# Performance work log

Hardware: AMD Instinct MI355X
Metric: run time of the kernel (lower is better)

The kernel has to match this reference:

```python
import jax, jax.numpy as jnp
import numpy as np

D_MODEL = 1024
NHEAD = 16
HEAD_DIM = D_MODEL // NHEAD
SCALE = 1.0 / float(np.sqrt(HEAD_DIM))


def setup_inputs() -> dict:
    key = jax.random.key(0)
    ks = jax.random.split(key, 9)
    B, S = 1, 4096
    s = 1.0 / float(np.sqrt(D_MODEL))
    inp = {
        "x": jax.random.normal(ks[0], (B, S, D_MODEL), dtype=jnp.float32),
        "Wq": jax.random.uniform(ks[1], (D_MODEL, D_MODEL), jnp.float32, -s, s),
        "bq": jax.random.uniform(ks[2], (D_MODEL,), jnp.float32, -s, s),
        "Wk": jax.random.uniform(ks[3], (D_MODEL, D_MODEL), jnp.float32, -s, s),
        "bk": jax.random.uniform(ks[4], (D_MODEL,), jnp.float32, -s, s),
        "Wv": jax.random.uniform(ks[5], (D_MODEL, D_MODEL), jnp.float32, -s, s),
        "bv": jax.random.uniform(ks[6], (D_MODEL,), jnp.float32, -s, s),
        "Wo": jax.random.uniform(ks[7], (D_MODEL, D_MODEL), jnp.float32, -s, s),
        "bo": jax.random.uniform(ks[8], (D_MODEL,), jnp.float32, -s, s),
    }
    return inp


def reference(x, Wq, bq, Wk, bk, Wv, bv, Wo, bo):
    B, S, _ = x.shape
    # projections (torch Linear: y = x @ W.T + b)
    q = x @ Wq.T + bq
    k = x @ Wk.T + bk
    v = x @ Wv.T + bv
    # [B, H, S, Dh]
    q = q.reshape(B, S, NHEAD, HEAD_DIM).transpose(0, 2, 1, 3)
    k = k.reshape(B, S, NHEAD, HEAD_DIM).transpose(0, 2, 1, 3)
    v = v.reshape(B, S, NHEAD, HEAD_DIM).transpose(0, 2, 1, 3)
    # [B, H, S, S] scores with causal mask
    scores = jnp.einsum("bhsd,bhtd->bhst", q, k) * SCALE
    causal = jnp.triu(jnp.ones((S, S), dtype=bool), k=1)
    scores = jnp.where(causal, -jnp.inf, scores)
    attn = jax.nn.softmax(scores, axis=-1)
    out = jnp.einsum("bhst,bhtd->bhsd", attn, v)
    out = out.transpose(0, 2, 1, 3).reshape(B, S, D_MODEL)
    return out @ Wo.T + bo
```

## Files before the change

kernel.cpp:

```cpp
#include <hip/hip_runtime.h>

typedef unsigned short u16;
typedef unsigned int u32;
typedef short bf16x8 __attribute__((ext_vector_type(8)));
typedef float f32x4 __attribute__((ext_vector_type(4)));
typedef float f32x16 __attribute__((ext_vector_type(16)));
typedef u32 u32x4 __attribute__((ext_vector_type(4)));

#define S_LEN 4096
#define DM 1024
#define NH 16
#define DH 64
#define CE 0.18033688f
#define THR 8.0f

typedef const __attribute__((address_space(1))) u32 gu32;
typedef __attribute__((address_space(3))) u32 lu32;

#define EXP2(x) __builtin_amdgcn_exp2f(x)

__device__ __forceinline__ u16 f2bf(float f) {
  u32 u = __builtin_bit_cast(u32, f);
  u += 0x7fff + ((u >> 16) & 1);
  return (u16)(u >> 16);
}

__device__ __forceinline__ f32x16 zero16() {
  f32x16 z;
#pragma unroll
  for (int i = 0; i < 16; ++i) z[i] = 0.f;
  return z;
}

__device__ __forceinline__ u32 cvt_pk_bf16(float lo, float hi) {
  u32 r;
  asm("v_cvt_pk_bf16_f32 %0, %1, %2" : "=v"(r) : "v"(lo), "v"(hi));
  return r;
}

__device__ __forceinline__ void pl_swap(u32& a, u32& b) {
  asm("v_permlane32_swap_b32 %0, %1" : "+v"(a), "+v"(b));
}

__global__ void cvt_bf16(const float* __restrict__ in, u16* __restrict__ out, int n4) {
  int i = blockIdx.x * blockDim.x + threadIdx.x;
  if (i < n4) {
    float4 v = ((const float4*)in)[i];
    ushort4 o;
    o.x = f2bf(v.x); o.y = f2bf(v.y); o.z = f2bf(v.z); o.w = f2bf(v.w);
    ((ushort4*)out)[i] = o;
  }
}

__global__ void cvt_bf16_w4(const float* __restrict__ a, const float* __restrict__ b,
                            const float* __restrict__ c, const float* __restrict__ d,
                            u16* __restrict__ oa, u16* __restrict__ ob2,
                            u16* __restrict__ oc, u16* __restrict__ od, int n4) {
  const int w = blockIdx.y;
  const float* src = (w == 0) ? a : (w == 1) ? b : (w == 2) ? c : d;
  u16* dst = (w == 0) ? oa : (w == 1) ? ob2 : (w == 2) ? oc : od;
  int i = blockIdx.x * blockDim.x + threadIdx.x;
  if (i < n4) {
    float4 v = ((const float4*)src)[i];
    ushort4 o;
    o.x = f2bf(v.x); o.y = f2bf(v.y); o.z = f2bf(v.z); o.w = f2bf(v.w);
    ((ushort4*)dst)[i] = o;
  }
}

__global__ __launch_bounds__(256) void gemm_qkv(const u16* __restrict__ A,
                                                const u16* __restrict__ Wq_, const u16* __restrict__ Wk_, const u16* __restrict__ Wv_,
                                                const float* __restrict__ bq_, const float* __restrict__ bk_, const float* __restrict__ bv_,
                                                u16* __restrict__ Qo, u16* __restrict__ Ko, u16* __restrict__ Vo) {
  __shared__ __align__(16) u16 As[128 * 32];
  __shared__ __align__(16) u16 Bs[128 * 32];
  const int z = blockIdx.z;
  const u16* Bt = (z == 0) ? Wq_ : (z == 1) ? Wk_ : Wv_;
  const float* bias = (z == 0) ? bq_ : (z == 1) ? bk_ : bv_;

  const int tid = threadIdx.x;
  const int lane = tid & 63;
  const int wid = tid >> 6;
  const int wm = wid >> 1, wn = wid & 1;
  const int bm = blockIdx.x * 128, bn = blockIdx.y * 128;
  const int lr = lane & 15, lg = lane >> 4;

  f32x4 acc[4][4];
#pragma unroll
  for (int i = 0; i < 4; ++i)
#pragma unroll
    for (int j = 0; j < 4; ++j) acc[i][j] = f32x4{0.f, 0.f, 0.f, 0.f};

  const int r0 = tid >> 2;
  const int c0 = (tid & 3) * 8;
  const u16* ga0 = A + (size_t)(bm + r0) * DM + c0;
  const u16* gb0 = Bt + (size_t)(bn + r0) * DM + c0;

  for (int kt = 0; kt < DM; kt += 32) {
    __builtin_amdgcn_global_load_lds((gu32*)(ga0 + kt),            (lu32*)(As + tid * 8),        16, 0, 0);
    __builtin_amdgcn_global_load_lds((gu32*)(ga0 + 64 * DM + kt),  (lu32*)(As + 2048 + tid * 8), 16, 0, 0);
    __builtin_amdgcn_global_load_lds((gu32*)(gb0 + kt),            (lu32*)(Bs + tid * 8),        16, 0, 0);
    __builtin_amdgcn_global_load_lds((gu32*)(gb0 + 64 * DM + kt),  (lu32*)(Bs + 2048 + tid * 8), 16, 0, 0);
    __syncthreads();
    bf16x8 af[4], bfr[4];
#pragma unroll
    for (int i = 0; i < 4; ++i) af[i] = *(const bf16x8*)&As[(wm * 64 + i * 16 + lr) * 32 + lg * 8];
#pragma unroll
    for (int j = 0; j < 4; ++j) bfr[j] = *(const bf16x8*)&Bs[(wn * 64 + j * 16 + lr) * 32 + lg * 8];
#pragma unroll
    for (int i = 0; i < 4; ++i)
#pragma unroll
      for (int j = 0; j < 4; ++j)
        acc[i][j] = __builtin_amdgcn_mfma_f32_16x16x32_bf16(af[i], bfr[j], acc[i][j], 0, 0, 0);
    __syncthreads();
  }

#pragma unroll
  for (int i = 0; i < 4; ++i) {
    const int row = bm + wm * 64 + i * 16 + lg * 4;
#pragma unroll
    for (int j = 0; j < 4; ++j) {
      const int col = bn + wn * 64 + j * 16 + lr;
      const float b = bias[col];
#pragma unroll
      for (int r = 0; r < 4; ++r) {
        const float v = acc[i][j][r] + b;
        const int s = row + r;
        if (z == 0) {
          Qo[(size_t)s * DM + col] = f2bf(v * CE);
        } else if (z == 1) {
          const int hh = col >> 6, c = col & 63;
          Ko[(size_t)hh * (S_LEN * 64) + (size_t)(s >> 5) * 2048 +
             (c >> 4) * 512 + ((c >> 3) & 1) * 256 + (s & 31) * 8 + (c & 7)] = f2bf(v);
        } else {
          const int hh = col >> 6, dl = col & 63;
          const int kl = s & 31;
          Vo[(size_t)hh * (S_LEN * 64) + (size_t)(s >> 5) * 2048 +
             ((dl >> 5) * 2 + (kl >> 4)) * 512 +
             ((((kl >> 3) & 1) * 32 + (dl & 31)) * 8) + (kl & 7)] = f2bf(v);
        }
      }
    }
  }
}

__global__ __launch_bounds__(256) void gemm_out(const u16* __restrict__ A,
                                                const u16* __restrict__ Bt,
                                                const float* __restrict__ bias,
                                                float* __restrict__ Cp) {
  __shared__ __align__(16) u16 As[128 * 32];
  __shared__ __align__(16) u16 Bs[128 * 32];
  const int tid = threadIdx.x;
  const int lane = tid & 63;
  const int wid = tid >> 6;
  const int wm = wid >> 1, wn = wid & 1;
  const int bm = blockIdx.x * 128, bn = blockIdx.y * 128;
  const int lr = lane & 15, lg = lane >> 4;

  f32x4 acc[4][4];
#pragma unroll
  for (int i = 0; i < 4; ++i)
#pragma unroll
    for (int j = 0; j < 4; ++j) acc[i][j] = f32x4{0.f, 0.f, 0.f, 0.f};

  const int r0 = tid >> 2;
  const int c0 = (tid & 3) * 8;
  const u16* ga0 = A + (size_t)(bm + r0) * DM + c0;
  const u16* gb0 = Bt + (size_t)(bn + r0) * DM + c0;

  for (int kt = 0; kt < DM; kt += 32) {
    __builtin_amdgcn_global_load_lds((gu32*)(ga0 + kt),            (lu32*)(As + tid * 8),        16, 0, 0);
    __builtin_amdgcn_global_load_lds((gu32*)(ga0 + 64 * DM + kt),  (lu32*)(As + 2048 + tid * 8), 16, 0, 0);
    __builtin_amdgcn_global_load_lds((gu32*)(gb0 + kt),            (lu32*)(Bs + tid * 8),        16, 0, 0);
    __builtin_amdgcn_global_load_lds((gu32*)(gb0 + 64 * DM + kt),  (lu32*)(Bs + 2048 + tid * 8), 16, 0, 0);
    __syncthreads();
    bf16x8 af[4], bfr[4];
#pragma unroll
    for (int i = 0; i < 4; ++i) af[i] = *(const bf16x8*)&As[(wm * 64 + i * 16 + lr) * 32 + lg * 8];
#pragma unroll
    for (int j = 0; j < 4; ++j) bfr[j] = *(const bf16x8*)&Bs[(wn * 64 + j * 16 + lr) * 32 + lg * 8];
#pragma unroll
    for (int i = 0; i < 4; ++i)
#pragma unroll
      for (int j = 0; j < 4; ++j)
        acc[i][j] = __builtin_amdgcn_mfma_f32_16x16x32_bf16(af[i], bfr[j], acc[i][j], 0, 0, 0);
    __syncthreads();
  }

#pragma unroll
  for (int i = 0; i < 4; ++i) {
    const int row = bm + wm * 64 + i * 16 + lg * 4;
#pragma unroll
    for (int j = 0; j < 4; ++j) {
      const int col = bn + wn * 64 + j * 16 + lr;
      const float b = bias[col];
#pragma unroll
      for (int r = 0; r < 4; ++r)
        Cp[(size_t)(row + r) * DM + col] = acc[i][j][r] + b;
    }
  }
}


__device__ __forceinline__ void ld_kt(const u16* __restrict__ tb, bf16x8* kf) {
  kf[0] = *(const bf16x8*)&tb[0];
  kf[1] = *(const bf16x8*)&tb[512];
  kf[2] = *(const bf16x8*)&tb[1024];
  kf[3] = *(const bf16x8*)&tb[1536];
}

template<bool DIAG>
__device__ __forceinline__ void attn_tile32(const bf16x8* kf, const bf16x8* vf,
                                            const bf16x8* qf, int lld,
                                            f32x16& o0, f32x16& o1,
                                            float& m, float& lsum) {
  f32x16 s = zero16();
  __builtin_amdgcn_s_setprio(1);
  s = __builtin_amdgcn_mfma_f32_32x32x16_bf16(kf[0], qf[0], s, 0, 0, 0);
  s = __builtin_amdgcn_mfma_f32_32x32x16_bf16(kf[1], qf[1], s, 0, 0, 0);
  s = __builtin_amdgcn_mfma_f32_32x32x16_bf16(kf[2], qf[2], s, 0, 0, 0);
  s = __builtin_amdgcn_mfma_f32_32x32x16_bf16(kf[3], qf[3], s, 0, 0, 0);
  __builtin_amdgcn_s_setprio(0);

  float p[16];
#pragma unroll
  for (int r = 0; r < 16; ++r) {
    const int kl = (r & 3) + 8 * (r >> 2);
    p[r] = (!DIAG || kl <= lld) ? s[r] : -1e30f;
  }
  float t[8];
#pragma unroll
  for (int i = 0; i < 8; ++i) t[i] = fmaxf(p[i], p[i + 8]);
#pragma unroll
  for (int i = 0; i < 4; ++i) t[i] = fmaxf(t[i], t[i + 4]);
  float mx = fmaxf(fmaxf(t[0], t[1]), fmaxf(t[2], t[3]));
  mx = fmaxf(mx, __shfl_xor(mx, 32));

  if (!__all(mx <= m + THR)) {
    const float mn = fmaxf(m, mx);
    const float al = EXP2(m - mn);
    m = mn;
    lsum *= al;
    o0 *= al;
    o1 *= al;
  }
#pragma unroll
  for (int r = 0; r < 16; ++r) p[r] = EXP2(p[r] - m);
  float st[8];
#pragma unroll
  for (int i = 0; i < 8; ++i) st[i] = p[i] + p[i + 8];
#pragma unroll
  for (int i = 0; i < 4; ++i) st[i] = st[i] + st[i + 4];
  lsum += (st[0] + st[1]) + (st[2] + st[3]);

  u32 w0 = cvt_pk_bf16(p[0],  p[1]);
  u32 w1 = cvt_pk_bf16(p[2],  p[3]);
  u32 w2 = cvt_pk_bf16(p[4],  p[5]);
  u32 w3 = cvt_pk_bf16(p[6],  p[7]);
  u32 w4 = cvt_pk_bf16(p[8],  p[9]);
  u32 w5 = cvt_pk_bf16(p[10], p[11]);
  u32 w6 = cvt_pk_bf16(p[12], p[13]);
  u32 w7 = cvt_pk_bf16(p[14], p[15]);
  pl_swap(w0, w2);
  pl_swap(w1, w3);
  pl_swap(w4, w6);
  pl_swap(w5, w7);
  const bf16x8 pb0 = __builtin_bit_cast(bf16x8, u32x4{w0, w1, w2, w3});
  const bf16x8 pb1 = __builtin_bit_cast(bf16x8, u32x4{w4, w5, w6, w7});

  __builtin_amdgcn_s_setprio(1);
  o0 = __builtin_amdgcn_mfma_f32_32x32x16_bf16(vf[0], pb0, o0, 0, 0, 0);
  o0 = __builtin_amdgcn_mfma_f32_32x32x16_bf16(vf[1], pb1, o0, 0, 0, 0);
  o1 = __builtin_amdgcn_mfma_f32_32x32x16_bf16(vf[2], pb0, o1, 0, 0, 0);
  o1 = __builtin_amdgcn_mfma_f32_32x32x16_bf16(vf[3], pb1, o1, 0, 0, 0);
  __builtin_amdgcn_s_setprio(0);
}

__device__ __forceinline__ void attn_tile64(const bf16x8* kA, const bf16x8* kB,
                                            const bf16x8* vA, const bf16x8* vB,
                                            const bf16x8* qf,
                                            f32x16& o0, f32x16& o1,
                                            float& m, float& lsum) {
  f32x16 s0 = zero16(), s1 = zero16();
  __builtin_amdgcn_s_setprio(1);
  s0 = __builtin_amdgcn_mfma_f32_32x32x16_bf16(kA[0], qf[0], s0, 0, 0, 0);
  s1 = __builtin_amdgcn_mfma_f32_32x32x16_bf16(kB[0], qf[0], s1, 0, 0, 0);
  s0 = __builtin_amdgcn_mfma_f32_32x32x16_bf16(kA[1], qf[1], s0, 0, 0, 0);
  s1 = __builtin_amdgcn_mfma_f32_32x32x16_bf16(kB[1], qf[1], s1, 0, 0, 0);
  s0 = __builtin_amdgcn_mfma_f32_32x32x16_bf16(kA[2], qf[2], s0, 0, 0, 0);
  s1 = __builtin_amdgcn_mfma_f32_32x32x16_bf16(kB[2], qf[2], s1, 0, 0, 0);
  s0 = __builtin_amdgcn_mfma_f32_32x32x16_bf16(kA[3], qf[3], s0, 0, 0, 0);
  s1 = __builtin_amdgcn_mfma_f32_32x32x16_bf16(kB[3], qf[3], s1, 0, 0, 0);
  __builtin_amdgcn_s_setprio(0);

  float t[16];
#pragma unroll
  for (int i = 0; i < 16; ++i) t[i] = fmaxf(s0[i], s1[i]);
#pragma unroll
  for (int i = 0; i < 8; ++i) t[i] = fmaxf(t[i], t[i + 8]);
#pragma unroll
  for (int i = 0; i < 4; ++i) t[i] = fmaxf(t[i], t[i + 4]);
  float mx = fmaxf(fmaxf(t[0], t[1]), fmaxf(t[2], t[3]));
  mx = fmaxf(mx, __shfl_xor(mx, 32));

  if (!__all(mx <= m + THR)) {
    const float mn = fmaxf(m, mx);
    const float al = EXP2(m - mn);
    m = mn;
    lsum *= al;
    o0 *= al;
    o1 *= al;
  }
  float p0[16], p1[16];
#pragma unroll
  for (int r = 0; r < 16; ++r) p0[r] = EXP2(s0[r] - m);
#pragma unroll
  for (int r = 0; r < 16; ++r) p1[r] = EXP2(s1[r] - m);
  float st[16];
#pragma unroll
  for (int i = 0; i < 16; ++i) st[i] = p0[i] + p1[i];
#pragma unroll
  for (int i = 0; i < 8; ++i) st[i] = st[i] + st[i + 8];
#pragma unroll
  for (int i = 0; i < 4; ++i) st[i] = st[i] + st[i + 4];
  lsum += (st[0] + st[1]) + (st[2] + st[3]);

  u32 a0 = cvt_pk_bf16(p0[0],  p0[1]);
  u32 a1 = cvt_pk_bf16(p0[2],  p0[3]);
  u32 a2 = cvt_pk_bf16(p0[4],  p0[5]);
  u32 a3 = cvt_pk_bf16(p0[6],  p0[7]);
  u32 a4 = cvt_pk_bf16(p0[8],  p0[9]);
  u32 a5 = cvt_pk_bf16(p0[10], p0[11]);
  u32 a6 = cvt_pk_bf16(p0[12], p0[13]);
  u32 a7 = cvt_pk_bf16(p0[14], p0[15]);
  pl_swap(a0, a2); pl_swap(a1, a3); pl_swap(a4, a6); pl_swap(a5, a7);
  const bf16x8 pb0A = __builtin_bit_cast(bf16x8, u32x4{a0, a1, a2, a3});
  const bf16x8 pb1A = __builtin_bit_cast(bf16x8, u32x4{a4, a5, a6, a7});
  u32 b0 = cvt_pk_bf16(p1[0],  p1[1]);
  u32 b1 = cvt_pk_bf16(p1[2],  p1[3]);
  u32 b2 = cvt_pk_bf16(p1[4],  p1[5]);
  u32 b3 = cvt_pk_bf16(p1[6],  p1[7]);
  u32 b4 = cvt_pk_bf16(p1[8],  p1[9]);
  u32 b5 = cvt_pk_bf16(p1[10], p1[11]);
  u32 b6 = cvt_pk_bf16(p1[12], p1[13]);
  u32 b7 = cvt_pk_bf16(p1[14], p1[15]);
  pl_swap(b0, b2); pl_swap(b1, b3); pl_swap(b4, b6); pl_swap(b5, b7);
  const bf16x8 pb0B = __builtin_bit_cast(bf16x8, u32x4{b0, b1, b2, b3});
  const bf16x8 pb1B = __builtin_bit_cast(bf16x8, u32x4{b4, b5, b6, b7});

  __builtin_amdgcn_s_setprio(1);
  o0 = __builtin_amdgcn_mfma_f32_32x32x16_bf16(vA[0], pb0A, o0, 0, 0, 0);
  o1 = __builtin_amdgcn_mfma_f32_32x32x16_bf16(vA[2], pb0A, o1, 0, 0, 0);
  o0 = __builtin_amdgcn_mfma_f32_32x32x16_bf16(vA[1], pb1A, o0, 0, 0, 0);
  o1 = __builtin_amdgcn_mfma_f32_32x32x16_bf16(vA[3], pb1A, o1, 0, 0, 0);
  o0 = __builtin_amdgcn_mfma_f32_32x32x16_bf16(vB[0], pb0B, o0, 0, 0, 0);
  o1 = __builtin_amdgcn_mfma_f32_32x32x16_bf16(vB[2], pb0B, o1, 0, 0, 0);
  o0 = __builtin_amdgcn_mfma_f32_32x32x16_bf16(vB[1], pb1B, o0, 0, 0, 0);
  o1 = __builtin_amdgcn_mfma_f32_32x32x16_bf16(vB[3], pb1B, o1, 0, 0, 0);
  __builtin_amdgcn_s_setprio(0);
}

__device__ __forceinline__ void run_strip(int strip, int h, int wv, int lane,
                                          int ll, int hi, int lld,
                                          const u16* __restrict__ Q, const u16* __restrict__ Kp,
                                          const u16* __restrict__ Vp, u16* __restrict__ O,
                                          float (*ms)[64], float (*ls)[64],
                                          float (*ob)[64][33]) {
  const int wqb = strip * 32;
  const u16* qrow = Q + (size_t)(wqb + ll) * DM + h * DH + hi * 8;
  bf16x8 qf[4];
#pragma unroll
  for (int d = 0; d < 4; ++d) qf[d] = *(const bf16x8*)&qrow[d * 16];

  const u16* Kb = Kp + (size_t)h * (S_LEN * 64) + lane * 8;
  const u16* Vb = Vp + (size_t)h * (S_LEN * 64) + lane * 8;

  f32x16 o0 = zero16(), o1 = zero16();
  float m = -1e30f, lsum = 0.f;

  const int ntot = strip + 1;
  const int base = ntot >> 2, rem = ntot & 3;
  const int cnt = base + ((wv >= 4 - rem) ? 1 : 0);
  const int ex = wv - (4 - rem);
  const int start = wv * base + (ex > 0 ? ex : 0);
  const int end = start + cnt;

  if (cnt > 0) {
    bf16x8 kA[4], kB[4], vA[4], vB[4];
    const int endND = (wv == 3) ? end - 1 : end;
    int t = start;
    for (; t + 2 <= endND; t += 2) {
      ld_kt(Kb + (size_t)t * 2048, kA);
      ld_kt(Kb + (size_t)(t + 1) * 2048, kB);
      ld_kt(Vb + (size_t)t * 2048, vA);
      ld_kt(Vb + (size_t)(t + 1) * 2048, vB);
      attn_tile64(kA, kB, vA, vB, qf, o0, o1, m, lsum);
    }
    if (t < endND) {
      ld_kt(Kb + (size_t)t * 2048, kA);
      ld_kt(Vb + (size_t)t * 2048, vA);
      attn_tile32<false>(kA, vA, qf, lld, o0, o1, m, lsum);
      ++t;
    }
    if (wv == 3) {
      ld_kt(Kb + (size_t)(end - 1) * 2048, kA);
      ld_kt(Vb + (size_t)(end - 1) * 2048, vA);
      attn_tile32<true>(kA, vA, qf, lld, o0, o1, m, lsum);
    }
  }

  if (wv == 1 || wv == 3) {
    const int slot = wv >> 1;
    ms[slot][lane] = m;
    ls[slot][lane] = lsum;
#pragma unroll
    for (int j = 0; j < 16; ++j) ob[slot][lane][j] = o0[j];
#pragma unroll
    for (int j = 0; j < 16; ++j) ob[slot][lane][16 + j] = o1[j];
  }
  __syncthreads();
  if (wv == 0 || wv == 2) {
    const int slot = wv >> 1;
    const float m2 = ms[slot][lane], l2 = ls[slot][lane];
    const float M = fmaxf(m, m2);
    const float a = EXP2(m - M);
    const float b = EXP2(m2 - M);
    lsum = lsum * a + l2 * b;
#pragma unroll
    for (int j = 0; j < 16; ++j) o0[j] = o0[j] * a + ob[slot][lane][j] * b;
#pragma unroll
    for (int j = 0; j < 16; ++j) o1[j] = o1[j] * a + ob[slot][lane][16 + j] * b;
    m = M;
  }
  __syncthreads();
  if (wv == 2) {
    ms[1][lane] = m;
    ls[1][lane] = lsum;
#pragma unroll
    for (int j = 0; j < 16; ++j) ob[1][lane][j] = o0[j];
#pragma unroll
    for (int j = 0; j < 16; ++j) ob[1][lane][16 + j] = o1[j];
  }
  __syncthreads();
  if (wv == 0) {
    const float m2 = ms[1][lane], l2 = ls[1][lane];
    const float M = fmaxf(m, m2);
    const float a = EXP2(m - M);
    const float b = EXP2(m2 - M);
    float lf = lsum * a + l2 * b;
#pragma unroll
    for (int j = 0; j < 16; ++j) o0[j] = o0[j] * a + ob[1][lane][j] * b;
#pragma unroll
    for (int j = 0; j < 16; ++j) o1[j] = o1[j] * a + ob[1][lane][16 + j] * b;
    lf += __shfl_xor(lf, 32);
    const float inv = 1.f / lf;
    u16* orow = O + (size_t)(wqb + ll) * DM + h * DH;
#pragma unroll
    for (int g2 = 0; g2 < 4; ++g2) {
      ushort4 oa;
      oa.x = f2bf(o0[g2 * 4 + 0] * inv); oa.y = f2bf(o0[g2 * 4 + 1] * inv);
      oa.z = f2bf(o0[g2 * 4 + 2] * inv); oa.w = f2bf(o0[g2 * 4 + 3] * inv);
      *(ushort4*)&orow[g2 * 8 + hi * 4] = oa;
      ushort4 obv;
      obv.x = f2bf(o1[g2 * 4 + 0] * inv); obv.y = f2bf(o1[g2 * 4 + 1] * inv);
      obv.z = f2bf(o1[g2 * 4 + 2] * inv); obv.w = f2bf(o1[g2 * 4 + 3] * inv);
      *(ushort4*)&orow[32 + g2 * 8 + hi * 4] = obv;
    }
  }
  __syncthreads();
}

__global__ __launch_bounds__(256) void attn_fwd12(const u16* __restrict__ Q,
                                                  const u16* __restrict__ Kp,
                                                  const u16* __restrict__ Vp,
                                                  u16* __restrict__ O) {
  __shared__ float ms[2][64];
  __shared__ float ls[2][64];
  __shared__ float ob[2][64][33];

  const int tid = threadIdx.x;
  const int lane = tid & 63;
  const int wv = tid >> 6;
  const int ll = lane & 31, hi = lane >> 5;
  const int lld = ll - 4 * hi;
  const int bid = blockIdx.x;
  const int xcd = bid & 7;
  const int h = xcd * 2 + ((bid >> 3) & 1);
  const int pr = bid >> 4;

  run_strip(127 - pr, h, wv, lane, ll, hi, lld, Q, Kp, Vp, O, ms, ls, ob);
  run_strip(pr,       h, wv, lane, ll, hi, lld, Q, Kp, Vp, O, ms, ls, ob);
}

extern "C" void kernel_launch(void* const* d_in, const int* in_sizes, int n_in,
                              void* d_out, int out_size, void* d_ws, size_t ws_size,
                              hipStream_t stream) {
  const float* x  = (const float*)d_in[0];
  const float* Wq = (const float*)d_in[1];
  const float* bq = (const float*)d_in[2];
  const float* Wk = (const float*)d_in[3];
  const float* bk = (const float*)d_in[4];
  const float* Wv = (const float*)d_in[5];
  const float* bv = (const float*)d_in[6];
  const float* Wo = (const float*)d_in[7];
  const float* bo = (const float*)d_in[8];
  float* out = (float*)d_out;

  u16* xb  = (u16*)d_ws;
  u16* wqb = xb  + (size_t)S_LEN * DM;
  u16* wkb = wqb + (size_t)DM * DM;
  u16* wvb = wkb + (size_t)DM * DM;
  u16* wob = wvb + (size_t)DM * DM;
  u16* qbf = wob + (size_t)DM * DM;
  u16* kbf = qbf + (size_t)S_LEN * DM;
  u16* vtb = kbf + (size_t)S_LEN * DM;
  u16* obf = vtb + (size_t)S_LEN * DM;

  cvt_bf16<<<(S_LEN * DM / 4 + 255) / 256, 256, 0, stream>>>(x, xb, S_LEN * DM / 4);
  cvt_bf16_w4<<<dim3((DM * DM / 4 + 255) / 256, 4), 256, 0, stream>>>(
      Wq, Wk, Wv, Wo, wqb, wkb, wvb, wob, DM * DM / 4);

  gemm_qkv<<<dim3(S_LEN / 128, DM / 128, 3), 256, 0, stream>>>(
      xb, wqb, wkb, wvb, bq, bk, bv, qbf, kbf, vtb);

  attn_fwd12<<<dim3(1024), 256, 0, stream>>>(qbf, kbf, vtb, obf);

  gemm_out<<<dim3(S_LEN / 128, DM / 128), 256, 0, stream>>>(obf, wob, bo, out);
}
```

Before: 136.5 us.

## Split attention into one strip per block, shrink output GEMM tile, use 3-way max

```diff
diff --git a/kernel.cpp b/kernel.cpp
--- a/kernel.cpp
+++ b/kernel.cpp
@@ -40,6 +40,10 @@
 
 __device__ __forceinline__ void pl_swap(u32& a, u32& b) {
   asm("v_permlane32_swap_b32 %0, %1" : "+v"(a), "+v"(b));
+}
+
+__device__ __forceinline__ float f3(float a, float b, float c) {
+  return fmaxf(fmaxf(a, b), c);
 }
 
 __global__ void cvt_bf16(const float* __restrict__ in, u16* __restrict__ out, int n4) {
@@ -148,18 +152,18 @@
                                                 const u16* __restrict__ Bt,
                                                 const float* __restrict__ bias,
                                                 float* __restrict__ Cp) {
-  __shared__ __align__(16) u16 As[128 * 32];
+  __shared__ __align__(16) u16 As[64 * 32];
   __shared__ __align__(16) u16 Bs[128 * 32];
   const int tid = threadIdx.x;
   const int lane = tid & 63;
   const int wid = tid >> 6;
   const int wm = wid >> 1, wn = wid & 1;
-  const int bm = blockIdx.x * 128, bn = blockIdx.y * 128;
+  const int bm = blockIdx.x * 64, bn = blockIdx.y * 128;
   const int lr = lane & 15, lg = lane >> 4;
 
-  f32x4 acc[4][4];
-#pragma unroll
-  for (int i = 0; i < 4; ++i)
+  f32x4 acc[2][4];
+#pragma unroll
+  for (int i = 0; i < 2; ++i)
 #pragma unroll
     for (int j = 0; j < 4; ++j) acc[i][j] = f32x4{0.f, 0.f, 0.f, 0.f};
 
@@ -170,17 +174,16 @@
 
   for (int kt = 0; kt < DM; kt += 32) {
     __builtin_amdgcn_global_load_lds((gu32*)(ga0 + kt),            (lu32*)(As + tid * 8),        16, 0, 0);
-    __builtin_amdgcn_global_load_lds((gu32*)(ga0 + 64 * DM + kt),  (lu32*)(As + 2048 + tid * 8), 16, 0, 0);
     __builtin_amdgcn_global_load_lds((gu32*)(gb0 + kt),            (lu32*)(Bs + tid * 8),        16, 0, 0);
     __builtin_amdgcn_global_load_lds((gu32*)(gb0 + 64 * DM + kt),  (lu32*)(Bs + 2048 + tid * 8), 16, 0, 0);
     __syncthreads();
-    bf16x8 af[4], bfr[4];
-#pragma unroll
-    for (int i = 0; i < 4; ++i) af[i] = *(const bf16x8*)&As[(wm * 64 + i * 16 + lr) * 32 + lg * 8];
+    bf16x8 af[2], bfr[4];
+#pragma unroll
+    for (int i = 0; i < 2; ++i) af[i] = *(const bf16x8*)&As[(wm * 32 + i * 16 + lr) * 32 + lg * 8];
 #pragma unroll
     for (int j = 0; j < 4; ++j) bfr[j] = *(const bf16x8*)&Bs[(wn * 64 + j * 16 + lr) * 32 + lg * 8];
 #pragma unroll
-    for (int i = 0; i < 4; ++i)
+    for (int i = 0; i < 2; ++i)
 #pragma unroll
       for (int j = 0; j < 4; ++j)
         acc[i][j] = __builtin_amdgcn_mfma_f32_16x16x32_bf16(af[i], bfr[j], acc[i][j], 0, 0, 0);
@@ -188,8 +191,8 @@
   }
 
 #pragma unroll
-  for (int i = 0; i < 4; ++i) {
-    const int row = bm + wm * 64 + i * 16 + lg * 4;
+  for (int i = 0; i < 2; ++i) {
+    const int row = bm + wm * 32 + i * 16 + lg * 4;
 #pragma unroll
     for (int j = 0; j < 4; ++j) {
       const int col = bn + wn * 64 + j * 16 + lr;
@@ -228,12 +231,12 @@
     const int kl = (r & 3) + 8 * (r >> 2);
     p[r] = (!DIAG || kl <= lld) ? s[r] : -1e30f;
   }
-  float t[8];
-#pragma unroll
-  for (int i = 0; i < 8; ++i) t[i] = fmaxf(p[i], p[i + 8]);
-#pragma unroll
-  for (int i = 0; i < 4; ++i) t[i] = fmaxf(t[i], t[i + 4]);
-  float mx = fmaxf(fmaxf(t[0], t[1]), fmaxf(t[2], t[3]));
+  const float m1 = f3(p[0], p[1], p[2]);
+  const float m2 = f3(p[3], p[4], p[5]);
+  const float m3 = f3(p[6], p[7], p[8]);
+  const float m4 = f3(p[9], p[10], p[11]);
+  const float m5 = f3(p[12], p[13], p[14]);
+  float mx = fmaxf(f3(m1, m2, m3), f3(m4, m5, p[15]));
   mx = fmaxf(mx, __shfl_xor(mx, 32));
 
   if (!__all(mx <= m + THR)) {
@@ -296,11 +299,12 @@
   float t[16];
 #pragma unroll
   for (int i = 0; i < 16; ++i) t[i] = fmaxf(s0[i], s1[i]);
-#pragma unroll
-  for (int i = 0; i < 8; ++i) t[i] = fmaxf(t[i], t[i + 8]);
-#pragma unroll
-  for (int i = 0; i < 4; ++i) t[i] = fmaxf(t[i], t[i + 4]);
-  float mx = fmaxf(fmaxf(t[0], t[1]), fmaxf(t[2], t[3]));
+  const float m1 = f3(t[0], t[1], t[2]);
+  const float m2 = f3(t[3], t[4], t[5]);
+  const float m3 = f3(t[6], t[7], t[8]);
+  const float m4 = f3(t[9], t[10], t[11]);
+  const float m5 = f3(t[12], t[13], t[14]);
+  float mx = fmaxf(f3(m1, m2, m3), f3(m4, m5, t[15]));
   mx = fmaxf(mx, __shfl_xor(mx, 32));
 
   if (!__all(mx <= m + THR)) {
@@ -467,10 +471,9 @@
       *(ushort4*)&orow[32 + g2 * 8 + hi * 4] = obv;
     }
   }
-  __syncthreads();
-}
-
-__global__ __launch_bounds__(256) void attn_fwd12(const u16* __restrict__ Q,
+}
+
+__global__ __launch_bounds__(256) void attn_fwd13(const u16* __restrict__ Q,
                                                   const u16* __restrict__ Kp,
                                                   const u16* __restrict__ Vp,
                                                   u16* __restrict__ O) {
@@ -486,10 +489,9 @@
   const int bid = blockIdx.x;
   const int xcd = bid & 7;
   const int h = xcd * 2 + ((bid >> 3) & 1);
-  const int pr = bid >> 4;
-
-  run_strip(127 - pr, h, wv, lane, ll, hi, lld, Q, Kp, Vp, O, ms, ls, ob);
-  run_strip(pr,       h, wv, lane, ll, hi, lld, Q, Kp, Vp, O, ms, ls, ob);
+  const int strip = 127 - (bid >> 4);
+
+  run_strip(strip, h, wv, lane, ll, hi, lld, Q, Kp, Vp, O, ms, ls, ob);
 }
 
 extern "C" void kernel_launch(void* const* d_in, const int* in_sizes, int n_in,
@@ -523,7 +525,7 @@
   gemm_qkv<<<dim3(S_LEN / 128, DM / 128, 3), 256, 0, stream>>>(
       xb, wqb, wkb, wvb, bq, bk, bv, qbf, kbf, vtb);
 
-  attn_fwd12<<<dim3(1024), 256, 0, stream>>>(qbf, kbf, vtb, obf);
-
-  gemm_out<<<dim3(S_LEN / 128, DM / 128), 256, 0, stream>>>(obf, wob, bo, out);
-}
+  attn_fwd13<<<dim3(2048), 256, 0, stream>>>(qbf, kbf, vtb, obf);
+
+  gemm_out<<<dim3(S_LEN / 64, DM / 128), 256, 0, stream>>>(obf, wob, bo, out);
+}
```

After: 132.2 us. 3.1% less time.
